# Optimization experiments

Hardware: AMD Instinct MI355X
Metric: run time of the kernel (lower is better)

Reference implementation:

```python
import jax, jax.numpy as jnp
import numpy as np

B = 4096      # number of query nodes (len(samp_neighs))
U = 50000     # number of unique sampled neighbor nodes
D = 300       # node feature dim (GloVe-style ConceptNet embeddings)
E = 131072    # total (node, neighbor) pairs, avg degree ~32


def setup_inputs() -> dict:
    key = jax.random.key(0)
    k1, k2, k3 = jax.random.split(key, 3)
    row_idx = jnp.sort(jax.random.randint(k1, (E,), 0, B, dtype=jnp.int64 if jax.config.jax_enable_x64 else jnp.int32)).astype(jnp.int32)
    col_idx = jax.random.randint(k2, (E,), 0, U).astype(jnp.int32)
    embed_matrix = jax.random.normal(k3, (U, D), dtype=jnp.float32)
    return {"row_idx": row_idx, "col_idx": col_idx, "embed_matrix": embed_matrix}


def reference(row_idx, col_idx, embed_matrix):
    # Build dense neighbor-membership mask [B, U]; .set (not .add) mirrors the
    # original's set semantics (duplicate neighbors count once).
    mask = jnp.zeros((B, U), dtype=embed_matrix.dtype).at[row_idx, col_idx].set(1.0)
    num_neigh = mask.sum(axis=1, keepdims=True)            # [B, 1]
    mask = mask / jnp.clip(num_neigh, 1e-8)                # row-normalize (mean)
    to_feats = mask @ embed_matrix                         # [B, D] mean aggregation
    return to_feats
```

## Files before the change

### kernel.cpp

```cpp
#include <hip/hip_runtime.h>


#define DFEAT 300
#define NCHUNK 75
#define COLS_CAP 1024

__global__ __launch_bounds__(64) void mean_agg_kernel(
    const int* __restrict__ row_idx,
    const int* __restrict__ col_idx,
    const float* __restrict__ embed,
    float* __restrict__ out,
    int E)
{
    const int b = blockIdx.x;
    const int t = threadIdx.x;

    int lo = 0, hi = E;
    while (lo < hi) { int m = (lo + hi) >> 1; if (row_idx[m] < b)     lo = m + 1; else hi = m; }
    const int start = lo;
    hi = E;
    while (lo < hi) { int m = (lo + hi) >> 1; if (row_idx[m] < b + 1) lo = m + 1; else hi = m; }
    const int end = lo;
    const int deg = end - start;

    __shared__ int s_cols[COLS_CAP];
    for (int k = t; k < deg && k < COLS_CAP; k += 64) s_cols[k] = col_idx[start + k];
    __syncthreads();

    float4 acc0 = {0.f, 0.f, 0.f, 0.f};
    float4 acc1 = {0.f, 0.f, 0.f, 0.f};
    int count = 0;

    for (int e = 0; e < deg; ++e) {
        const int c = (e < COLS_CAP) ? s_cols[e] : col_idx[start + e];
        int dup = 0;
        for (int i = t; i < e; i += 64) {
            const int ci = (i < COLS_CAP) ? s_cols[i] : col_idx[start + i];
            dup |= (ci == c);
        }
        if (!__any(dup)) {
            const float4* __restrict__ rowp =
                (const float4*)(embed + (long long)c * DFEAT);
            const float4 v0 = rowp[t];
            acc0.x += v0.x; acc0.y += v0.y; acc0.z += v0.z; acc0.w += v0.w;
            if (t < NCHUNK - 64) {
                const float4 v1 = rowp[t + 64];
                acc1.x += v1.x; acc1.y += v1.y; acc1.z += v1.z; acc1.w += v1.w;
            }
            ++count;
        }
    }

    const float scale = (count > 0) ? (1.0f / (float)count) : 0.0f;
    float4* __restrict__ orow = (float4*)(out + (long long)b * DFEAT);
    float4 r0; r0.x = acc0.x * scale; r0.y = acc0.y * scale;
               r0.z = acc0.z * scale; r0.w = acc0.w * scale;
    orow[t] = r0;
    if (t < NCHUNK - 64) {
        float4 r1; r1.x = acc1.x * scale; r1.y = acc1.y * scale;
                   r1.z = acc1.z * scale; r1.w = acc1.w * scale;
        orow[t + 64] = r1;
    }
}

extern "C" void kernel_launch(void* const* d_in, const int* in_sizes, int n_in,
                              void* d_out, int out_size, void* d_ws, size_t ws_size,
                              hipStream_t stream) {
    const int*   row_idx = (const int*)  d_in[0];
    const int*   col_idx = (const int*)  d_in[1];
    const float* embed   = (const float*)d_in[2];
    float*       out     = (float*)      d_out;

    const int E = in_sizes[0];
    const int B = out_size / DFEAT;

    mean_agg_kernel<<<B, 64, 0, stream>>>(row_idx, col_idx, embed, out, E);
}
```

Measured before the change: 124.8 us.

## Split neighbor gather across four waves with parallel dedup and shared reduction

Each block now uses four wavefronts. A parallel dedup pass builds a compacted list of unique neighbor columns in shared memory, replacing the serial per-edge ballot in the gather loop. The waves then gather disjoint subsets of rows, with two rows in flight per iteration, and combine their partial sums through shared memory before normalizing. This is meant to raise memory-level parallelism and remove the serialized dedup from the load path, at the cost of more shared memory, an extra barrier, and a unique list capped at 512 entries.

```diff
diff --git a/kernel.cpp b/kernel.cpp
--- a/kernel.cpp
+++ b/kernel.cpp
@@ -1,65 +1,98 @@
 #include <hip/hip_runtime.h>
 
 
-#define DFEAT 300
+#define DFEAT  300
 #define NCHUNK 75
-#define COLS_CAP 1024
+#define COLS_CAP 512
+#define NWAVE  4
 
-__global__ __launch_bounds__(64) void mean_agg_kernel(
+__global__ __launch_bounds__(256) void mean_agg_kernel(
     const int* __restrict__ row_idx,
     const int* __restrict__ col_idx,
     const float* __restrict__ embed,
     float* __restrict__ out,
     int E)
 {
-    const int b = blockIdx.x;
-    const int t = threadIdx.x;
+    const int b    = blockIdx.x;
+    const int tid  = threadIdx.x;
+    const int t    = tid & 63;
+    const int wave = tid >> 6;
 
     int lo = 0, hi = E;
     while (lo < hi) { int m = (lo + hi) >> 1; if (row_idx[m] < b)     lo = m + 1; else hi = m; }
     const int start = lo;
     hi = E;
     while (lo < hi) { int m = (lo + hi) >> 1; if (row_idx[m] < b + 1) lo = m + 1; else hi = m; }
-    const int end = lo;
-    const int deg = end - start;
+    const int deg = lo - start;
 
-    __shared__ int s_cols[COLS_CAP];
-    for (int k = t; k < deg && k < COLS_CAP; k += 64) s_cols[k] = col_idx[start + k];
+    __shared__ int   s_cols[COLS_CAP];
+    __shared__ int   s_uniq[COLS_CAP];
+    __shared__ int   s_cnt;
+    __shared__ float s_part[NWAVE][DFEAT];
+
+    if (tid == 0) s_cnt = 0;
+    for (int k = tid; k < deg && k < COLS_CAP; k += 256) s_cols[k] = col_idx[start + k];
     __syncthreads();
+
+    for (int k = tid; k < deg; k += 256) {
+        const int c = (k < COLS_CAP) ? s_cols[k] : col_idx[start + k];
+        bool dup = false;
+        for (int i = 0; i < k; ++i) {
+            const int ci = (i < COLS_CAP) ? s_cols[i] : col_idx[start + i];
+            dup |= (ci == c);
+        }
+        if (!dup) {
+            const int p = atomicAdd(&s_cnt, 1);
+            if (p < COLS_CAP) s_uniq[p] = c;
+        }
+    }
+    __syncthreads();
+    const int cnt = s_cnt;
 
     float4 acc0 = {0.f, 0.f, 0.f, 0.f};
     float4 acc1 = {0.f, 0.f, 0.f, 0.f};
-    int count = 0;
+    const bool hi_lane = (t < NCHUNK - 64);
 
-    for (int e = 0; e < deg; ++e) {
-        const int c = (e < COLS_CAP) ? s_cols[e] : col_idx[start + e];
-        int dup = 0;
-        for (int i = t; i < e; i += 64) {
-            const int ci = (i < COLS_CAP) ? s_cols[i] : col_idx[start + i];
-            dup |= (ci == c);
+    int u = wave;
+    for (; u + NWAVE < cnt; u += 2 * NWAVE) {
+        const float4* __restrict__ p0 = (const float4*)(embed + (long long)s_uniq[u] * DFEAT);
+        const float4* __restrict__ p1 = (const float4*)(embed + (long long)s_uniq[u + NWAVE] * DFEAT);
+        const float4 x0 = p0[t];
+        const float4 y0 = p1[t];
+        acc0.x += x0.x; acc0.y += x0.y; acc0.z += x0.z; acc0.w += x0.w;
+        acc0.x += y0.x; acc0.y += y0.y; acc0.z += y0.z; acc0.w += y0.w;
+        if (hi_lane) {
+            const float4 x1 = p0[t + 64];
+            const float4 y1 = p1[t + 64];
+            acc1.x += x1.x; acc1.y += x1.y; acc1.z += x1.z; acc1.w += x1.w;
+            acc1.x += y1.x; acc1.y += y1.y; acc1.z += y1.z; acc1.w += y1.w;
         }
-        if (!__any(dup)) {
-            const float4* __restrict__ rowp =
-                (const float4*)(embed + (long long)c * DFEAT);
-            const float4 v0 = rowp[t];
-            acc0.x += v0.x; acc0.y += v0.y; acc0.z += v0.z; acc0.w += v0.w;
-            if (t < NCHUNK - 64) {
-                const float4 v1 = rowp[t + 64];
-                acc1.x += v1.x; acc1.y += v1.y; acc1.z += v1.z; acc1.w += v1.w;
-            }
-            ++count;
+    }
+    if (u < cnt) {
+        const float4* __restrict__ p0 = (const float4*)(embed + (long long)s_uniq[u] * DFEAT);
+        const float4 x0 = p0[t];
+        acc0.x += x0.x; acc0.y += x0.y; acc0.z += x0.z; acc0.w += x0.w;
+        if (hi_lane) {
+            const float4 x1 = p0[t + 64];
+            acc1.x += x1.x; acc1.y += x1.y; acc1.z += x1.z; acc1.w += x1.w;
         }
     }
 
-    const float scale = (count > 0) ? (1.0f / (float)count) : 0.0f;
-    float4* __restrict__ orow = (float4*)(out + (long long)b * DFEAT);
-    float4 r0; r0.x = acc0.x * scale; r0.y = acc0.y * scale;
-               r0.z = acc0.z * scale; r0.w = acc0.w * scale;
-    orow[t] = r0;
-    if (t < NCHUNK - 64) {
-        float4 r1; r1.x = acc1.x * scale; r1.y = acc1.y * scale;
-                   r1.z = acc1.z * scale; r1.w = acc1.w * scale;
-        orow[t + 64] = r1;
+    *(float4*)&s_part[wave][4 * t] = acc0;
+    if (hi_lane) *(float4*)&s_part[wave][256 + 4 * t] = acc1;
+    __syncthreads();
+
+    if (tid < NCHUNK) {
+        const float scale = (cnt > 0) ? (1.0f / (float)cnt) : 0.0f;
+        const int o = 4 * tid;
+        float4 r = {0.f, 0.f, 0.f, 0.f};
+        #pragma unroll
+        for (int w = 0; w < NWAVE; ++w) {
+            const float4 p = *(const float4*)&s_part[w][o];
+            r.x += p.x; r.y += p.y; r.z += p.z; r.w += p.w;
+        }
+        r.x *= scale; r.y *= scale; r.z *= scale; r.w *= scale;
+        *(float4*)(out + (long long)b * DFEAT + o) = r;
     }
 }
 
@@ -74,5 +107,5 @@
     const int E = in_sizes[0];
     const int B = out_size / DFEAT;
 
-    mean_agg_kernel<<<B, 64, 0, stream>>>(row_idx, col_idx, embed, out, E);
+    mean_agg_kernel<<<B, 256, 0, stream>>>(row_idx, col_idx, embed, out, E);
 }
```

Result: faster. 121.7 us (-2.5%).
